# Optimization experiments

Measured on AMD Instinct MI355X. Metric: run time of the kernel, lower is better.

The kernel has to match this reference:

```python
import jax, jax.numpy as jnp
import numpy as np

D_MODEL = 1024
N_HEADS = 16
D_HEAD = D_MODEL // N_HEADS
RANK = 128
KNOW_RANK = 128
N_COMPRESS = 64
N_EXPAND = 32
N_KNOW = 16384
TOPK_C = 8
TOPK_E = 4
KNOW_K = 8
B, S = 8, 1024
EPS_LN = 1e-5


def setup_inputs() -> dict:
    key = jax.random.key(0)
    ks = jax.random.split(key, 16)
    inp = {
        'x': jax.random.normal(ks[0], (B, S, D_MODEL), jnp.float32),
        'importance': jax.random.uniform(ks[1], (B, S), jnp.float32),
        # routers, stored as [d_model, n] so out = x @ W
        'Wc': jax.random.normal(ks[2], (D_MODEL, N_COMPRESS), jnp.float32) * 0.02,
        'WQr': jax.random.normal(ks[3], (D_MODEL, N_EXPAND), jnp.float32) * 0.02,
        'WKr': jax.random.normal(ks[4], (D_MODEL, N_EXPAND), jnp.float32) * 0.02,
        'WVr': jax.random.normal(ks[5], (D_MODEL, N_EXPAND), jnp.float32) * 0.02,
        'Wm': jax.random.normal(ks[6], (D_MODEL, N_COMPRESS), jnp.float32) * 0.02,
        # shared neuron pools
        'compress_neurons': jax.random.normal(ks[7], (N_COMPRESS, D_MODEL, RANK), jnp.float32) / np.sqrt(D_MODEL),
        'expand_pool': jax.random.normal(ks[8], (N_EXPAND, RANK, D_MODEL), jnp.float32) / np.sqrt(RANK),
        'knowledge_K': jax.random.normal(ks[9], (N_KNOW, KNOW_RANK), jnp.float32) * 0.02,
        'knowledge_V': jax.random.normal(ks[10], (N_KNOW, D_MODEL), jnp.float32) * 0.02,
        # output projection stored as [d_in, d_out]
        'W_O': jax.random.normal(ks[11], (D_MODEL, D_MODEL), jnp.float32) / np.sqrt(D_MODEL),
        'ln1_s': jnp.ones((D_MODEL,), jnp.float32),
        'ln1_b': jnp.zeros((D_MODEL,), jnp.float32),
        'ln2_s': jnp.ones((D_MODEL,), jnp.float32),
        'ln2_b': jnp.zeros((D_MODEL,), jnp.float32),
    }
    return inp


def _layernorm(x, s, b):
    mu = jnp.mean(x, axis=-1, keepdims=True)
    var = jnp.mean(jnp.square(x - mu), axis=-1, keepdims=True)
    return (x - mu) * jax.lax.rsqrt(var + EPS_LN) * s + b


def _topk_sparsify(w, k):
    # w: [B, n] -> sparse renormalized weights [B, n]
    vals, idx = jax.lax.top_k(w, k)
    rows = jnp.arange(w.shape[0])[:, None]
    sparse = jnp.zeros_like(w).at[rows, idx].set(vals)
    return sparse / (jnp.sum(sparse, axis=-1, keepdims=True) + 1e-8)


def _route(nx, importance, W, k):
    pref = jax.nn.softmax(jnp.einsum('bsd,dn->bsn', nx, W), axis=-1)
    dense = jnp.einsum('bs,bsn->bn', importance, pref)
    return _topk_sparsify(dense, k)


def _forward(x, importance, Wc, WQr, WKr, WVr, Wm, compress_neurons,
             expand_pool, knowledge_K, knowledge_V, W_O, ln1_s, ln1_b, ln2_s, ln2_b):
    Bx, Sx, D = x.shape
    n1 = _layernorm(x, ln1_s, ln1_b)

    # --- attention routing ---
    cw = _route(n1, importance, Wc, TOPK_C)
    ewQ = _route(n1, importance, WQr, TOPK_E)
    ewK = _route(n1, importance, WKr, TOPK_E)
    ewV = _route(n1, importance, WVr, TOPK_E)

    # --- synthesized low-rank attention weights ---
    shared_compress = jnp.einsum('bn,ndr->bdr', cw, compress_neurons)
    h = jnp.einsum('bsd,bdr->bsr', n1, shared_compress)
    EQ = jnp.einsum('bn,nrd->brd', ewQ, expand_pool)
    EK = jnp.einsum('bn,nrd->brd', ewK, expand_pool)
    EV = jnp.einsum('bn,nrd->brd', ewV, expand_pool)
    Q = jnp.einsum('bsr,brd->bsd', h, EQ).reshape(Bx, Sx, N_HEADS, D_HEAD).transpose(0, 2, 1, 3)
    K = jnp.einsum('bsr,brd->bsd', h, EK).reshape(Bx, Sx, N_HEADS, D_HEAD).transpose(0, 2, 1, 3)
    V = jnp.einsum('bsr,brd->bsd', h, EV).reshape(Bx, Sx, N_HEADS, D_HEAD).transpose(0, 2, 1, 3)

    scores = jnp.einsum('bhqd,bhkd->bhqk', Q, K) / np.sqrt(D_HEAD)
    causal = jnp.tril(jnp.ones((Sx, Sx), bool))
    scores = jnp.where(causal, scores, jnp.finfo(scores.dtype).min)
    attn = jax.nn.softmax(scores, axis=-1)
    attn_out = jnp.einsum('bhqk,bhkd->bhqd', attn, V).transpose(0, 2, 1, 3).reshape(Bx, Sx, D)
    attn_out = attn_out @ W_O
    x = x + attn_out

    # --- memory ---
    n2 = _layernorm(x, ln2_s, ln2_b)
    mw = _route(n2, importance, Wm, TOPK_C)
    sc_m = jnp.einsum('bn,ndr->bdr', mw, compress_neurons)
    Qm = jnp.einsum('bsd,bdr->bsr', n2, sc_m)  # knowledge_rank == rank -> no query_proj
    mscores = jnp.einsum('bsr,nr->bsn', Qm, knowledge_K) / np.sqrt(KNOW_RANK)
    topv, topi = jax.lax.top_k(mscores, KNOW_K)
    w = jax.nn.softmax(topv, axis=-1)  # [B,S,k]
    selV = knowledge_V[topi]  # [B,S,k,D]
    mem_out = jnp.einsum('bsk,bskd->bsd', w, selV)
    return x + mem_out


def reference(x, importance, Wc, WQr, WKr, WVr, Wm, compress_neurons,
              expand_pool, knowledge_K, knowledge_V, W_O, ln1_s, ln1_b, ln2_s, ln2_b):
    return _forward(x, importance, Wc, WQr, WKr, WVr, Wm, compress_neurons,
                    expand_pool, knowledge_K, knowledge_V, W_O, ln1_s, ln1_b, ln2_s, ln2_b)
```

## Files before the change

kernel.cpp:

```cpp
#include <hip/hip_runtime.h>
#include <hip/hip_bf16.h>

#define BD 8
#define SD 1024
#define DM 1024
#define NH 16
#define DH 64
#define RK 128
#define NK 16384

typedef __attribute__((ext_vector_type(8))) short bf16x8;
typedef __attribute__((ext_vector_type(4))) float f32x4;

__device__ __forceinline__ unsigned short f2b(float f) {
    unsigned u = __float_as_uint(f);
    unsigned r = (u + 0x7FFFu + ((u >> 16) & 1u)) >> 16;
    return (unsigned short)r;
}
__device__ __forceinline__ float b2f(unsigned short h) {
    return __uint_as_float(((unsigned)h) << 16);
}

__global__ void __launch_bounds__(256) ln_kernel(const float* __restrict__ x,
                                                 const float* __restrict__ sc,
                                                 const float* __restrict__ bi,
                                                 unsigned short* __restrict__ outh,
                                                 unsigned short* __restrict__ outl) {
    const int tok = blockIdx.x;
    __shared__ float xs[DM];
    __shared__ float red[256];
    const float* xp = x + (size_t)tok * DM;
    float s = 0.f;
    for (int i = threadIdx.x; i < DM; i += 256) { float v = xp[i]; xs[i] = v; s += v; }
    red[threadIdx.x] = s; __syncthreads();
    for (int st = 128; st; st >>= 1) { if (threadIdx.x < st) red[threadIdx.x] += red[threadIdx.x + st]; __syncthreads(); }
    float mu = red[0] * (1.f / DM);
    __syncthreads();
    float vs = 0.f;
    for (int i = threadIdx.x; i < DM; i += 256) { float d = xs[i] - mu; vs += d * d; }
    red[threadIdx.x] = vs; __syncthreads();
    for (int st = 128; st; st >>= 1) { if (threadIdx.x < st) red[threadIdx.x] += red[threadIdx.x + st]; __syncthreads(); }
    float rs = rsqrtf(red[0] * (1.f / DM) + 1e-5f);
    for (int i = threadIdx.x; i < DM; i += 256) {
        float v = (xs[i] - mu) * rs * sc[i] + bi[i];
        unsigned short h = f2b(v);
        outh[(size_t)tok * DM + i] = h;
        outl[(size_t)tok * DM + i] = f2b(v - b2f(h));
    }
}

__global__ void __launch_bounds__(256) concatw_kernel(const float* __restrict__ Wc,
                                                      const float* __restrict__ WQr,
                                                      const float* __restrict__ WKr,
                                                      const float* __restrict__ WVr,
                                                      const float* __restrict__ Wm,
                                                      unsigned short* __restrict__ WTh,
                                                      unsigned short* __restrict__ WTl) {
    const int i = blockIdx.x * 256 + threadIdx.x;
    const int c = i >> 10, d = i & 1023;
    float v = 0.f;
    if (c < 64)       v = Wc[d * 64 + c];
    else if (c < 96)  v = WQr[d * 32 + c - 64];
    else if (c < 128) v = WKr[d * 32 + c - 96];
    else if (c < 160) v = WVr[d * 32 + c - 128];
    else if (c >= 192) v = Wm[d * 64 + c - 192];
    unsigned short h = f2b(v);
    WTh[i] = h;
    WTl[i] = f2b(v - b2f(h));
}

__global__ void __launch_bounds__(256) gemm_split(const unsigned short* __restrict__ Ah,
                                                  const unsigned short* __restrict__ Al,
                                                  const unsigned short* __restrict__ Bh,
                                                  const unsigned short* __restrict__ Bl,
                                                  float* __restrict__ C,
                                                  int N, int K) {
    const int row0 = blockIdx.y * 128, col0 = blockIdx.x * 64;
    const int t = threadIdx.x;
    const int w = t >> 6, l = t & 63, lq = l & 15, lg = l >> 4;
    __shared__ unsigned short sAh[128 * 64];
    __shared__ unsigned short sAl[128 * 64];
    __shared__ unsigned short sBh[64 * 64];
    __shared__ unsigned short sBl[64 * 64];
    f32x4 acc[2][4];
    #pragma unroll
    for (int mi = 0; mi < 2; mi++)
        #pragma unroll
        for (int ni = 0; ni < 4; ni++) acc[mi][ni] = f32x4{0.f, 0.f, 0.f, 0.f};

    for (int k0 = 0; k0 < K; k0 += 64) {
        __syncthreads();
        #pragma unroll
        for (int p = 0; p < 4; p++) {
            const int e = t * 8 + p * 2048;
            const int row = e >> 6, col = e & 63;
            const int sw = (e * 2) ^ ((row & 7) << 4);
            *(bf16x8*)((char*)sAh + sw) = *(const bf16x8*)(Ah + (size_t)(row0 + row) * K + k0 + col);
            *(bf16x8*)((char*)sAl + sw) = *(const bf16x8*)(Al + (size_t)(row0 + row) * K + k0 + col);
        }
        #pragma unroll
        for (int p = 0; p < 2; p++) {
            const int e = t * 8 + p * 2048;
            const int row = e >> 6, col = e & 63;
            const int sw = (e * 2) ^ ((row & 7) << 4);
            *(bf16x8*)((char*)sBh + sw) = *(const bf16x8*)(Bh + (size_t)(col0 + row) * K + k0 + col);
            *(bf16x8*)((char*)sBl + sw) = *(const bf16x8*)(Bl + (size_t)(col0 + row) * K + k0 + col);
        }
        __syncthreads();
        #pragma unroll
        for (int kk = 0; kk < 2; kk++) {
            bf16x8 ah[2], al[2], bh[4], bl[4];
            #pragma unroll
            for (int mi = 0; mi < 2; mi++) {
                const int r = w * 32 + mi * 16 + lq;
                const int off = (r * 128 + lg * 16 + kk * 64) ^ ((r & 7) << 4);
                ah[mi] = *(const bf16x8*)((const char*)sAh + off);
                al[mi] = *(const bf16x8*)((const char*)sAl + off);
            }
            #pragma unroll
            for (int ni = 0; ni < 4; ni++) {
                const int r = ni * 16 + lq;
                const int off = (r * 128 + lg * 16 + kk * 64) ^ ((r & 7) << 4);
                bh[ni] = *(const bf16x8*)((const char*)sBh + off);
                bl[ni] = *(const bf16x8*)((const char*)sBl + off);
            }
            #pragma unroll
            for (int mi = 0; mi < 2; mi++)
                #pragma unroll
                for (int ni = 0; ni < 4; ni++) {
                    acc[mi][ni] = __builtin_amdgcn_mfma_f32_16x16x32_bf16(ah[mi], bh[ni], acc[mi][ni], 0, 0, 0);
                    acc[mi][ni] = __builtin_amdgcn_mfma_f32_16x16x32_bf16(ah[mi], bl[ni], acc[mi][ni], 0, 0, 0);
                    acc[mi][ni] = __builtin_amdgcn_mfma_f32_16x16x32_bf16(al[mi], bh[ni], acc[mi][ni], 0, 0, 0);
                }
        }
    }
    #pragma unroll
    for (int mi = 0; mi < 2; mi++)
        #pragma unroll
        for (int j = 0; j < 4; j++) {
            const int row = row0 + w * 32 + mi * 16 + lg * 4 + j;
            #pragma unroll
            for (int ni = 0; ni < 4; ni++)
                C[(size_t)row * N + col0 + ni * 16 + lq] = acc[mi][ni][j];
        }
}

__global__ void __launch_bounds__(256) softpref_kernel(const float* __restrict__ lgt,
                                                       const float* __restrict__ imp,
                                                       float* __restrict__ wpref) {
    const int tok = blockIdx.x * 64 + (threadIdx.x >> 2);
    const int sg = threadIdx.x & 3;
    const int o = (sg == 0) ? 0 : (64 + 32 * (sg - 1));
    const int n = (sg == 0) ? 64 : 32;
    const float* lp = lgt + (size_t)tok * 192 + o;
    float m = -1e30f;
    for (int i = 0; i < n; i++) m = fmaxf(m, lp[i]);
    float ss = 0.f;
    for (int i = 0; i < n; i++) ss += __expf(lp[i] - m);
    const float scl = imp[tok] / ss;
    float* wp = wpref + (size_t)tok * 160 + o;
    for (int i = 0; i < n; i++) wp[i] = __expf(lp[i] - m) * scl;
}

__global__ void __launch_bounds__(256) softm_kernel(const float* __restrict__ lgt,
                                                    const float* __restrict__ imp,
                                                    float* __restrict__ wpref) {
    const int tok = blockIdx.x * 256 + threadIdx.x;
    const float* lp = lgt + (size_t)tok * 64;
    float m = -1e30f;
    for (int i = 0; i < 64; i++) m = fmaxf(m, lp[i]);
    float ss = 0.f;
    for (int i = 0; i < 64; i++) ss += __expf(lp[i] - m);
    const float scl = imp[tok] / ss;
    for (int i = 0; i < 64; i++) wpref[(size_t)tok * 64 + i] = __expf(lp[i] - m) * scl;
}

__global__ void __launch_bounds__(256) reduce_pref(const float* __restrict__ wpref,
                                                   float* __restrict__ dense,
                                                   int ncols, int outoff) {
    const int b = blockIdx.x / ncols, c = blockIdx.x % ncols;
    __shared__ float red[256];
    float s = 0.f;
    for (int si = threadIdx.x; si < SD; si += 256)
        s += wpref[((size_t)(b * SD + si)) * ncols + c];
    red[threadIdx.x] = s; __syncthreads();
    for (int st = 128; st; st >>= 1) { if (threadIdx.x < st) red[threadIdx.x] += red[threadIdx.x + st]; __syncthreads(); }
    if (threadIdx.x == 0) dense[b * 224 + outoff + c] = red[0];
}

__global__ void topk_kernel(const float* __restrict__ dense,
                            int* __restrict__ ridx, float* __restrict__ rw,
                            int r0, int nr) {
    const int t = threadIdx.x;
    if (t >= BD * nr) return;
    const int b = t / nr, r = r0 + (t % nr);
    const int offs[5] = {0, 64, 96, 128, 160};
    const int ns[5]   = {64, 32, 32, 32, 64};
    const int ks[5]   = {8, 4, 4, 4, 8};
    const float* dv = dense + b * 224 + offs[r];
    const int n = ns[r], k = ks[r];
    unsigned long long mask = 0;
    float vals[8]; int idxs[8];
    float ssum = 0.f;
    for (int kk = 0; kk < k; kk++) {
        float best = -1e30f; int bi = 0;
        for (int i = 0; i < n; i++)
            if (!((mask >> i) & 1ull) && dv[i] > best) { best = dv[i]; bi = i; }
        mask |= 1ull << bi;
        vals[kk] = best; idxs[kk] = bi; ssum += best;
    }
    float inv = 1.f / (ssum + 1e-8f);
    for (int kk = 0; kk < 8; kk++) {
        ridx[(b * 5 + r) * 8 + kk] = (kk < k) ? idxs[kk] : 0;
        rw[(b * 5 + r) * 8 + kk]   = (kk < k) ? vals[kk] * inv : 0.f;
    }
}

__global__ void __launch_bounds__(256) combine_t_kernel(const float* __restrict__ pool,
                                                        const int* __restrict__ ridx,
                                                        const float* __restrict__ rw,
                                                        int router, int kc,
                                                        unsigned short* __restrict__ outT,
                                                        int Rp, int Cp) {
    const int b = blockIdx.z;
    const int r0 = blockIdx.y * 64, c0 = blockIdx.x * 64;
    __shared__ float ls[64][65];
    const int* ii = ridx + (b * 5 + router) * 8;
    const float* ww = rw + (b * 5 + router) * 8;
    const int t = threadIdx.x;
    const int rr = t >> 4, cc = (t & 15) * 4;
    #pragma unroll
    for (int p = 0; p < 4; p++) {
        const int r = rr + p * 16;
        float4 acc = {0.f, 0.f, 0.f, 0.f};
        for (int kk = 0; kk < kc; kk++) {
            const float w = ww[kk];
            float4 v = *(const float4*)&pool[((size_t)ii[kk] * Rp + r0 + r) * Cp + c0 + cc];
            acc.x += w * v.x; acc.y += w * v.y; acc.z += w * v.z; acc.w += w * v.w;
        }
        ls[r][cc] = acc.x; ls[r][cc + 1] = acc.y; ls[r][cc + 2] = acc.z; ls[r][cc + 3] = acc.w;
    }
    __syncthreads();
    unsigned short* op = outT + (size_t)b * Rp * Cp;
    #pragma unroll
    for (int q = 0; q < 2; q++) {
        const int c = (t >> 3) + q * 32;
        const int r8 = (t & 7) * 8;
        union { unsigned short s[8]; bf16x8 v; } u;
        #pragma unroll
        for (int j = 0; j < 8; j++) u.s[j] = f2b(ls[r8 + j][c]);
        *(bf16x8*)(op + (size_t)(c0 + c) * Rp + r0 + r8) = u.v;
    }
}

__global__ void __launch_bounds__(256) tcvt_kernel(const float* __restrict__ src,
                                                   unsigned short* __restrict__ dst,
                                                   int R, int Cc) {
    __shared__ float ls[64][65];
    const int r0 = blockIdx.y * 64, c0 = blockIdx.x * 64;
    const int t = threadIdx.x;
    #pragma unroll
    for (int p = 0; p < 16; p++) {
        const int e = p * 256 + t;
        const int r = e >> 6, c = e & 63;
        ls[r][c] = src[(size_t)(r0 + r) * Cc + c0 + c];
    }
    __syncthreads();
    #pragma unroll
    for (int p = 0; p < 16; p++) {
        const int e = p * 256 + t;
        const int c = e >> 6, r = e & 63;
        dst[(size_t)(c0 + c) * R + r0 + r] = f2b(ls[r][c]);
    }
}

__global__ void __launch_bounds__(256) cvt_bf16_kernel(const float* __restrict__ src,
                                                       unsigned short* __restrict__ dst,
                                                       float scale, int n4) {
    const int i = blockIdx.x * 256 + threadIdx.x;
    if (i >= n4) return;
    float4 v = ((const float4*)src)[i];
    unsigned r0 = (unsigned)f2b(v.x * scale) | ((unsigned)f2b(v.y * scale) << 16);
    unsigned r1 = (unsigned)f2b(v.z * scale) | ((unsigned)f2b(v.w * scale) << 16);
    uint2 o; o.x = r0; o.y = r1;
    ((uint2*)dst)[i] = o;
}

template<int OUTB, int HASX>
__global__ void __launch_bounds__(256) gemm_bf16(const unsigned short* __restrict__ A,
                                                 const unsigned short* __restrict__ Bt,
                                                 const float* __restrict__ X,
                                                 void* __restrict__ Cv,
                                                 int M, int N, int K,
                                                 long long sA, long long sB, long long sC) {
    const int bz = blockIdx.z;
    const unsigned short* Ab = A + (size_t)bz * sA;
    const unsigned short* Btb = Bt + (size_t)bz * sB;
    const int row0 = blockIdx.y * 128, col0 = blockIdx.x * 128;
    const int t = threadIdx.x;
    const int w = t >> 6, l = t & 63, lq = l & 15, lg = l >> 4;
    const int wr = w >> 1, wc = w & 1;
    __shared__ unsigned short As[128 * 64];
    __shared__ unsigned short Bs[128 * 64];
    f32x4 acc[4][4];
    #pragma unroll
    for (int mi = 0; mi < 4; mi++)
        #pragma unroll
        for (int ni = 0; ni < 4; ni++) acc[mi][ni] = f32x4{0.f, 0.f, 0.f, 0.f};

    for (int k0 = 0; k0 < K; k0 += 64) {
        __syncthreads();
        #pragma unroll
        for (int p = 0; p < 4; p++) {
            const int e = t * 8 + p * 2048;
            const int row = e >> 6, col = e & 63;
            bf16x8 va = *(const bf16x8*)(Ab + (size_t)(row0 + row) * K + k0 + col);
            *(bf16x8*)((char*)As + ((row * 128 + col * 2) ^ ((row & 7) << 4))) = va;
            bf16x8 vb = *(const bf16x8*)(Btb + (size_t)(col0 + row) * K + k0 + col);
            *(bf16x8*)((char*)Bs + ((row * 128 + col * 2) ^ ((row & 7) << 4))) = vb;
        }
        __syncthreads();
        #pragma unroll
        for (int kk = 0; kk < 2; kk++) {
            bf16x8 af[4], bg[4];
            #pragma unroll
            for (int mi = 0; mi < 4; mi++) {
                const int r = wr * 64 + mi * 16 + lq;
                af[mi] = *(const bf16x8*)((const char*)As + ((r * 128 + lg * 16 + kk * 64) ^ ((r & 7) << 4)));
            }
            #pragma unroll
            for (int ni = 0; ni < 4; ni++) {
                const int r = wc * 64 + ni * 16 + lq;
                bg[ni] = *(const bf16x8*)((const char*)Bs + ((r * 128 + lg * 16 + kk * 64) ^ ((r & 7) << 4)));
            }
            #pragma unroll
            for (int mi = 0; mi < 4; mi++)
                #pragma unroll
                for (int ni = 0; ni < 4; ni++)
                    acc[mi][ni] = __builtin_amdgcn_mfma_f32_16x16x32_bf16(af[mi], bg[ni], acc[mi][ni], 0, 0, 0);
        }
    }
    #pragma unroll
    for (int mi = 0; mi < 4; mi++) {
        #pragma unroll
        for (int j = 0; j < 4; j++) {
            const int row = row0 + wr * 64 + mi * 16 + lg * 4 + j;
            #pragma unroll
            for (int ni = 0; ni < 4; ni++) {
                const int col = col0 + wc * 64 + ni * 16 + lq;
                float v = acc[mi][ni][j];
                if (HASX) v += X[(size_t)row * N + col];
                if (OUTB) ((unsigned short*)Cv)[(size_t)bz * sC + (size_t)row * N + col] = f2b(v);
                else      ((float*)Cv)[(size_t)bz * sC + (size_t)row * N + col] = v;
            }
        }
    }
}

#define SWZV(d) (((((d) >> 1) ^ ((d) >> 3)) & 7) << 4)
__global__ void __launch_bounds__(256) attn_mfma_kernel(const unsigned short* __restrict__ Q,
                                                        const unsigned short* __restrict__ K,
                                                        const unsigned short* __restrict__ V,
                                                        unsigned short* __restrict__ O) {
    const int qt = blockIdx.x, hh = blockIdx.y, b = blockIdx.z;
    const int t = threadIdx.x;
    const int w = t >> 6, l = t & 63, lq = l & 15, lg = l >> 4;

    __shared__ unsigned short ks[2][64 * 64];
    __shared__ unsigned short vt[2][64 * 64];
    __shared__ unsigned short pl[4][16 * 64];

    const size_t base = (size_t)b * SD * DM + (size_t)hh * DH;
    const int qA = qt;
    const int qB = 15 - qt;

    bf16x8 aqA[2], aqB[2];
    {
        const unsigned short* qp = Q + base + (size_t)(qA * 64 + w * 16 + lq) * DM + lg * 8;
        aqA[0] = *(const bf16x8*)qp; aqA[1] = *(const bf16x8*)(qp + 32);
        const unsigned short* qp2 = Q + base + (size_t)(qB * 64 + w * 16 + lq) * DM + lg * 8;
        aqB[0] = *(const bf16x8*)qp2; aqB[1] = *(const bf16x8*)(qp2 + 32);
    }

    f32x4 oA[4], oB[4];
    #pragma unroll
    for (int dt = 0; dt < 4; dt++) { oA[dt] = f32x4{0.f,0.f,0.f,0.f}; oB[dt] = f32x4{0.f,0.f,0.f,0.f}; }
    float mA[4] = {-1e30f,-1e30f,-1e30f,-1e30f}, sA[4] = {0.f,0.f,0.f,0.f};
    float mB[4] = {-1e30f,-1e30f,-1e30f,-1e30f}, sB[4] = {0.f,0.f,0.f,0.f};

    const int ntile = 16 - qt;
    const int srow = t >> 3;
    const int scol = (t & 7) * 8;

    int cur = 0;

    #pragma unroll
    for (int p = 0; p < 2; p++) {
        const int row = srow + 32 * p;
        bf16x8 kv = *(const bf16x8*)(K + base + (size_t)row * DM + scol);
        *(bf16x8*)((char*)&ks[0][0] + ((row * 128 + scol * 2) ^ ((row & 7) << 4))) = kv;
        bf16x8 vv = *(const bf16x8*)(V + base + (size_t)row * DM + scol);
        #pragma unroll
        for (int j2 = 0; j2 < 8; j2++) {
            const int d = scol + j2;
            *(unsigned short*)((char*)&vt[0][0] + ((d * 128 + row * 2) ^ SWZV(d))) = (unsigned short)vv[j2];
        }
    }
    __syncthreads();

    auto compute = [&](int q0, const bf16x8* aq, f32x4* o_, float* m_, float* s_, int kt) {
        const f32x4 zero4 = {0.f, 0.f, 0.f, 0.f};
        f32x4 sacc[4];
        #pragma unroll
        for (int ct = 0; ct < 4; ct++) {
            const int krow = ct * 16 + lq;
            bf16x8 b0 = *(const bf16x8*)((const char*)&ks[cur][0] + ((krow * 128 + lg * 16) ^ ((lq & 7) << 4)));
            bf16x8 b1 = *(const bf16x8*)((const char*)&ks[cur][0] + ((krow * 128 + lg * 16 + 64) ^ ((lq & 7) << 4)));
            f32x4 s = __builtin_amdgcn_mfma_f32_16x16x32_bf16(aq[0], b0, zero4, 0, 0, 0);
            s = __builtin_amdgcn_mfma_f32_16x16x32_bf16(aq[1], b1, s, 0, 0, 0);
            sacc[ct] = s;
        }
        float tm[4];
        #pragma unroll
        for (int j = 0; j < 4; j++) {
            const int qg = q0 * 64 + w * 16 + lg * 4 + j;
            float mx = -1e30f;
            #pragma unroll
            for (int ct = 0; ct < 4; ct++) {
                const int kg = kt * 64 + ct * 16 + lq;
                float v = sacc[ct][j] * 0.125f;
                v = (kg <= qg) ? v : -1e30f;
                sacc[ct][j] = v;
                mx = fmaxf(mx, v);
            }
            #pragma unroll
            for (int d = 1; d < 16; d <<= 1) mx = fmaxf(mx, __shfl_xor(mx, d));
            tm[j] = mx;
        }
        #pragma unroll
        for (int j = 0; j < 4; j++) {
            const float nm = fmaxf(m_[j], tm[j]);
            const float so = __expf(m_[j] - nm);
            m_[j] = nm;
            float rs = 0.f;
            const int prow = lg * 4 + j;
            #pragma unroll
            for (int ct = 0; ct < 4; ct++) {
                const float p = __expf(sacc[ct][j] - nm);
                rs += p;
                const int byteoff = ((prow * 128) + (ct * 16 + lq) * 2) ^ ((prow & 7) << 4);
                *(unsigned short*)((char*)&pl[w][0] + byteoff) = f2b(p);
            }
            #pragma unroll
            for (int d = 1; d < 16; d <<= 1) rs += __shfl_xor(rs, d);
            s_[j] = s_[j] * so + rs;
            #pragma unroll
            for (int dt = 0; dt < 4; dt++) o_[dt][j] *= so;
        }
        asm volatile("s_waitcnt lgkmcnt(0)" ::: "memory");
        __builtin_amdgcn_sched_barrier(0);
        #pragma unroll
        for (int c = 0; c < 2; c++) {
            bf16x8 pa = *(const bf16x8*)((const char*)&pl[w][0] +
                          ((lq * 128 + lg * 16 + 64 * c) ^ ((lq & 7) << 4)));
            #pragma unroll
            for (int dt = 0; dt < 4; dt++) {
                const int dd = dt * 16 + lq;
                bf16x8 bv = *(const bf16x8*)((const char*)&vt[cur][0] +
                              ((dd * 128 + lg * 16 + 64 * c) ^ SWZV(dd)));
                o_[dt] = __builtin_amdgcn_mfma_f32_16x16x32_bf16(pa, bv, o_[dt], 0, 0, 0);
            }
        }
    };

    const int mymaxA = qA * 64 + w * 16 + 15;
    for (int kt = 0; kt < ntile; kt++) {
        bf16x8 kN[2], vN[2];
        const bool pre = (kt + 1 < ntile);
        if (pre) {
            #pragma unroll
            for (int p = 0; p < 2; p++) {
                const int row = srow + 32 * p;
                kN[p] = *(const bf16x8*)(K + base + (size_t)((kt + 1) * 64 + row) * DM + scol);
                vN[p] = *(const bf16x8*)(V + base + (size_t)((kt + 1) * 64 + row) * DM + scol);
            }
        }
        compute(qB, aqB, oB, mB, sB, kt);
        if (kt * 64 <= mymaxA) compute(qA, aqA, oA, mA, sA, kt);
        if (pre) {
            #pragma unroll
            for (int p = 0; p < 2; p++) {
                const int row = srow + 32 * p;
                *(bf16x8*)((char*)&ks[cur ^ 1][0] + ((row * 128 + scol * 2) ^ ((row & 7) << 4))) = kN[p];
                #pragma unroll
                for (int j2 = 0; j2 < 8; j2++) {
                    const int d = scol + j2;
                    *(unsigned short*)((char*)&vt[cur ^ 1][0] + ((d * 128 + row * 2) ^ SWZV(d))) =
                        (unsigned short)vN[p][j2];
                }
            }
        }
        __syncthreads();
        cur ^= 1;
    }

    #pragma unroll
    for (int j = 0; j < 4; j++) {
        const float invA = 1.f / sA[j];
        const float invB = 1.f / sB[j];
        const int rowA = qA * 64 + w * 16 + lg * 4 + j;
        const int rowB = qB * 64 + w * 16 + lg * 4 + j;
        unsigned short* opA = O + base + (size_t)rowA * DM;
        unsigned short* opB = O + base + (size_t)rowB * DM;
        #pragma unroll
        for (int dt = 0; dt < 4; dt++) {
            opA[dt * 16 + lq] = f2b(oA[dt][j] * invA);
            opB[dt * 16 + lq] = f2b(oB[dt][j] * invB);
        }
    }
}
#undef SWZV

#define CE(a, b) { float hi_ = fmaxf(a, b), lo_ = fminf(a, b); a = hi_; b = lo_; }
__global__ void __launch_bounds__(512, 4) know_score_kernel(const unsigned short* __restrict__ Qmb,
                                                            const unsigned short* __restrict__ kKb,
                                                            float* __restrict__ cand) {
    const int t = threadIdx.x;
    const int w = t >> 6, l = t & 63, lq = l & 15, lg = l >> 4;
    const int tok0 = blockIdx.x * 16;
    __shared__ unsigned short ks[8][16 * 128];

    bf16x8 aq[4];
    {
        const unsigned short* qp = Qmb + (size_t)(tok0 + lq) * 128 + lg * 8;
        #pragma unroll
        for (int c = 0; c < 4; c++) aq[c] = *(const bf16x8*)(qp + c * 32);
    }

    float L[4][8];
    #pragma unroll
    for (int j = 0; j < 4; j++)
        #pragma unroll
        for (int s = 0; s < 8; s++) L[j][s] = __uint_as_float(0xF2000000u | (unsigned)s);

    const unsigned short* gsrc = kKb + (((size_t)w * 2048) << 7) + l * 8;
    unsigned short* myks = &ks[w][0];

    bf16x8 vreg[4];
    #pragma unroll
    for (int p = 0; p < 4; p++) vreg[p] = *(const bf16x8*)(gsrc + p * 512);

    for (int t4 = 0; t4 < 32; t4++) {
        float B[4][4];
        #pragma unroll
        for (int sub = 0; sub < 4; sub++) {
            const int kt = t4 * 4 + sub;
            #pragma unroll
            for (int p = 0; p < 4; p++) {
                const int e = p * 512 + l * 8;
                const int row = e >> 7;
                *(bf16x8*)((char*)myks + ((e * 2) ^ ((row & 7) << 4))) = vreg[p];
            }
            if (kt < 127) {
                const unsigned short* src2 = gsrc + (size_t)(kt + 1) * 2048;
                #pragma unroll
                for (int p = 0; p < 4; p++) vreg[p] = *(const bf16x8*)(src2 + p * 512);
            }
            {
                const char* kb = (const char*)myks + lq * 256;
                const int sw = (lq & 7) << 4;
                f32x4 s = {0.f, 0.f, 0.f, 0.f};
                #pragma unroll
                for (int c = 0; c < 4; c++) {
                    bf16x8 bv = *(const bf16x8*)(kb + ((c * 64 + lg * 16) ^ sw));
                    s = __builtin_amdgcn_mfma_f32_16x16x32_bf16(aq[c], bv, s, 0, 0, 0);
                }
                const unsigned keyb = (unsigned)(w * 2048 + kt * 16 + lq);
                #pragma unroll
                for (int j = 0; j < 4; j++) {
                    unsigned u = __float_as_uint(s[j]);
                    B[j][sub] = __uint_as_float((u & 0xFFFFC000u) | keyb);
                }
            }
        }
        #pragma unroll
        for (int j = 0; j < 4; j++) {
            CE(B[j][0], B[j][2]); CE(B[j][1], B[j][3]);
            CE(B[j][0], B[j][1]); CE(B[j][2], B[j][3]);
            CE(B[j][1], B[j][2]);
            L[j][4] = fmaxf(L[j][4], B[j][3]);
            L[j][5] = fmaxf(L[j][5], B[j][2]);
            L[j][6] = fmaxf(L[j][6], B[j][1]);
            L[j][7] = fmaxf(L[j][7], B[j][0]);
            CE(L[j][0], L[j][4]); CE(L[j][1], L[j][5]); CE(L[j][2], L[j][6]); CE(L[j][3], L[j][7]);
            CE(L[j][0], L[j][2]); CE(L[j][1], L[j][3]); CE(L[j][4], L[j][6]); CE(L[j][5], L[j][7]);
            CE(L[j][0], L[j][1]); CE(L[j][2], L[j][3]); CE(L[j][4], L[j][5]); CE(L[j][6], L[j][7]);
        }
    }
    #pragma unroll
    for (int j = 0; j < 4; j++) {
        const int tok = tok0 + lg * 4 + j;
        float* cp = cand + ((size_t)tok << 10) + w * 128 + lq * 8;
        #pragma unroll
        for (int ss = 0; ss < 8; ss++) cp[ss] = L[j][ss];
    }
}
#undef CE

__global__ void __launch_bounds__(256) know_out_kernel(const float* __restrict__ cand,
                                                       const float* __restrict__ kV,
                                                       float* __restrict__ out) {
    const int t = threadIdx.x, w = t >> 6, l = t & 63;
    const int tok = blockIdx.x * 4 + w;
    const float* cp = cand + ((size_t)tok << 10);
    float lv[16];
    #pragma unroll
    for (int i = 0; i < 16; i++) lv[i] = cp[i * 64 + l];

    float topv[8]; int topi[8];
    #pragma unroll
    for (int kk = 0; kk < 8; kk++) {
        float m = lv[0];
        #pragma unroll
        for (int i = 1; i < 16; i++) m = fmaxf(m, lv[i]);
        #pragma unroll
        for (int d = 1; d < 64; d <<= 1) m = fmaxf(m, __shfl_xor(m, d));
        topv[kk] = m;
        topi[kk] = (int)(__float_as_uint(m) & 0x3FFFu);
        #pragma unroll
        for (int i = 0; i < 16; i++) lv[i] = (lv[i] == m) ? -1e31f : lv[i];
    }
    const float mx = topv[0];
    float e[8]; float ssum = 0.f;
    #pragma unroll
    for (int kk = 0; kk < 8; kk++) { e[kk] = __expf(topv[kk] - mx); ssum += e[kk]; }
    const float inv = 1.f / ssum;

    float4 acc[4];
    #pragma unroll
    for (int ch = 0; ch < 4; ch++) acc[ch] = float4{0.f, 0.f, 0.f, 0.f};
    #pragma unroll
    for (int kk = 0; kk < 8; kk++) {
        const float wk = e[kk] * inv;
        const float* vp = kV + ((size_t)topi[kk] << 10);
        #pragma unroll
        for (int ch = 0; ch < 4; ch++) {
            float4 v = *(const float4*)(vp + ch * 256 + l * 4);
            acc[ch].x += wk * v.x; acc[ch].y += wk * v.y;
            acc[ch].z += wk * v.z; acc[ch].w += wk * v.w;
        }
    }
    float* op = out + ((size_t)tok << 10);
    #pragma unroll
    for (int ch = 0; ch < 4; ch++) {
        float4 o = *(const float4*)(op + ch * 256 + l * 4);
        o.x += acc[ch].x; o.y += acc[ch].y; o.z += acc[ch].z; o.w += acc[ch].w;
        *(float4*)(op + ch * 256 + l * 4) = o;
    }
}

extern "C" void kernel_launch(void* const* d_in, const int* in_sizes, int n_in,
                              void* d_out, int out_size, void* d_ws, size_t ws_size,
                              hipStream_t stream) {
    const float* x    = (const float*)d_in[0];
    const float* imp  = (const float*)d_in[1];
    const float* Wc   = (const float*)d_in[2];
    const float* WQr  = (const float*)d_in[3];
    const float* WKr  = (const float*)d_in[4];
    const float* WVr  = (const float*)d_in[5];
    const float* Wm   = (const float*)d_in[6];
    const float* cneu = (const float*)d_in[7];
    const float* epool= (const float*)d_in[8];
    const float* kK   = (const float*)d_in[9];
    const float* kV   = (const float*)d_in[10];
    const float* WO   = (const float*)d_in[11];
    const float* ln1s = (const float*)d_in[12];
    const float* ln1b = (const float*)d_in[13];
    const float* ln2s = (const float*)d_in[14];
    const float* ln2b = (const float*)d_in[15];
    float* out = (float*)d_out;

    float* ws = (float*)d_ws;
    size_t o = 0;
    unsigned short* n1h = (unsigned short*)(ws + o); o += (size_t)BD * SD * DM / 2;
    unsigned short* n1l = (unsigned short*)(ws + o); o += (size_t)BD * SD * DM / 2;
    float* lgt   = ws + o; o += (size_t)BD * SD * 192;
    float* wpref = ws + o; o += (size_t)BD * SD * 160;
    float* dense = ws + o; o += (size_t)BD * 224;
    int*   ridx  = (int*)(ws + o); o += (size_t)BD * 5 * 8;
    float* rw    = ws + o; o += (size_t)BD * 5 * 8;
    unsigned short* WTh = (unsigned short*)(ws + o); o += (size_t)256 * 1024 / 2;
    unsigned short* WTl = (unsigned short*)(ws + o); o += (size_t)256 * 1024 / 2;
    unsigned short* scompT = (unsigned short*)(ws + o); o += (size_t)BD * RK * DM / 2;
    unsigned short* EQt = (unsigned short*)(ws + o); o += (size_t)BD * RK * DM / 2;
    unsigned short* EKt = (unsigned short*)(ws + o); o += (size_t)BD * RK * DM / 2;
    unsigned short* EVt = (unsigned short*)(ws + o); o += (size_t)BD * RK * DM / 2;
    unsigned short* hb  = (unsigned short*)(ws + o); o += (size_t)BD * SD * RK / 2;
    unsigned short* Qb16 = (unsigned short*)(ws + o); o += (size_t)BD * SD * DM / 2;
    unsigned short* Kb16 = (unsigned short*)(ws + o); o += (size_t)BD * SD * DM / 2;
    unsigned short* Vb16 = (unsigned short*)(ws + o); o += (size_t)BD * SD * DM / 2;
    unsigned short* attnb = (unsigned short*)(ws + o); o += (size_t)BD * SD * DM / 2;
    unsigned short* WOt = (unsigned short*)(ws + o); o += (size_t)DM * DM / 2;
    unsigned short* kKb = (unsigned short*)(ws + o); o += (size_t)NK * RK / 2;
    unsigned short* Qmb = (unsigned short*)(ws + o); o += (size_t)BD * SD * RK / 2;
    float* cand = ws + o; o += (size_t)BD * SD * 1024;

    const int NTOK = BD * SD;

    concatw_kernel<<<1024, 256, 0, stream>>>(Wc, WQr, WKr, WVr, Wm, WTh, WTl);
    tcvt_kernel<<<dim3(16, 16, 1), 256, 0, stream>>>(WO, WOt, DM, DM);
    cvt_bf16_kernel<<<(NK * RK / 4) / 256, 256, 0, stream>>>(kK, kKb, 0.0883883476483184f, NK * RK / 4);

    ln_kernel<<<NTOK, 256, 0, stream>>>(x, ln1s, ln1b, n1h, n1l);
    gemm_split<<<dim3(3, NTOK / 128), 256, 0, stream>>>(n1h, n1l, WTh, WTl, lgt, 192, DM);
    softpref_kernel<<<NTOK / 64, 256, 0, stream>>>(lgt, imp, wpref);
    reduce_pref<<<BD * 160, 256, 0, stream>>>(wpref, dense, 160, 0);
    topk_kernel<<<1, 64, 0, stream>>>(dense, ridx, rw, 0, 4);
    combine_t_kernel<<<dim3(2, 16, BD), 256, 0, stream>>>(cneu, ridx, rw, 0, 8, scompT, DM, RK);
    combine_t_kernel<<<dim3(16, 2, BD), 256, 0, stream>>>(epool, ridx, rw, 1, 4, EQt, RK, DM);
    combine_t_kernel<<<dim3(16, 2, BD), 256, 0, stream>>>(epool, ridx, rw, 2, 4, EKt, RK, DM);
    combine_t_kernel<<<dim3(16, 2, BD), 256, 0, stream>>>(epool, ridx, rw, 3, 4, EVt, RK, DM);
    gemm_bf16<1, 0><<<dim3(1, 8, BD), 256, 0, stream>>>(n1h, scompT, nullptr, hb,
        SD, RK, DM, (long long)SD * DM, (long long)RK * DM, (long long)SD * RK);
    gemm_bf16<1, 0><<<dim3(8, 8, BD), 256, 0, stream>>>(hb, EQt, nullptr, Qb16,
        SD, DM, RK, (long long)SD * RK, (long long)DM * RK, (long long)SD * DM);
    gemm_bf16<1, 0><<<dim3(8, 8, BD), 256, 0, stream>>>(hb, EKt, nullptr, Kb16,
        SD, DM, RK, (long long)SD * RK, (long long)DM * RK, (long long)SD * DM);
    gemm_bf16<1, 0><<<dim3(8, 8, BD), 256, 0, stream>>>(hb, EVt, nullptr, Vb16,
        SD, DM, RK, (long long)SD * RK, (long long)DM * RK, (long long)SD * DM);
    attn_mfma_kernel<<<dim3(8, NH, BD), 256, 0, stream>>>(Qb16, Kb16, Vb16, attnb);
    gemm_bf16<0, 1><<<dim3(8, 64, 1), 256, 0, stream>>>(attnb, WOt, x, out,
        NTOK, DM, DM, 0, 0, 0);

    ln_kernel<<<NTOK, 256, 0, stream>>>(out, ln2s, ln2b, n1h, n1l);
    gemm_split<<<dim3(1, NTOK / 128), 256, 0, stream>>>(n1h, n1l,
        WTh + (size_t)192 * 1024, WTl + (size_t)192 * 1024, lgt, 64, DM);
    softm_kernel<<<NTOK / 256, 256, 0, stream>>>(lgt, imp, wpref);
    reduce_pref<<<BD * 64, 256, 0, stream>>>(wpref, dense, 64, 160);
    topk_kernel<<<1, 64, 0, stream>>>(dense, ridx, rw, 4, 1);
    combine_t_kernel<<<dim3(2, 16, BD), 256, 0, stream>>>(cneu, ridx, rw, 4, 8, scompT, DM, RK);
    gemm_bf16<1, 0><<<dim3(1, 8, BD), 256, 0, stream>>>(n1h, scompT, nullptr, Qmb,
        SD, RK, DM, (long long)SD * DM, (long long)RK * DM, (long long)SD * RK);
    know_score_kernel<<<NTOK / 16, 512, 0, stream>>>(Qmb, kKb, cand);
    know_out_kernel<<<NTOK / 4, 256, 0, stream>>>(cand, kV, out);
}
```

Measured before the change: 689.1 us.

## Fuse Q/K/V expand GEMMs into one and add narrow-tile GEMM for rank-128 projections

The three expand matrices are written side by side into one buffer, so a single batched GEMM produces an interleaved QKV tensor with a 3072-wide row stride. The attention kernel takes a leading-dimension argument to read from it. A dedicated 64x128-tile kernel replaces the generic GEMM for the two N=128 compress projections, giving 16 blocks per batch instead of 8. The aim is fewer launches and better occupancy on the skinny GEMMs, at the cost of strided Q/K/V reads in attention.

```diff
diff --git a/kernel.cpp b/kernel.cpp
--- a/kernel.cpp
+++ b/kernel.cpp
@@ -221,7 +221,7 @@
                                                         const float* __restrict__ rw,
                                                         int router, int kc,
                                                         unsigned short* __restrict__ outT,
-                                                        int Rp, int Cp) {
+                                                        int Rp, int Cp, long long sOut) {
     const int b = blockIdx.z;
     const int r0 = blockIdx.y * 64, c0 = blockIdx.x * 64;
     __shared__ float ls[64][65];
@@ -241,7 +241,7 @@
         ls[r][cc] = acc.x; ls[r][cc + 1] = acc.y; ls[r][cc + 2] = acc.z; ls[r][cc + 3] = acc.w;
     }
     __syncthreads();
-    unsigned short* op = outT + (size_t)b * Rp * Cp;
+    unsigned short* op = outT + (size_t)b * sOut;
     #pragma unroll
     for (int q = 0; q < 2; q++) {
         const int c = (t >> 3) + q * 32;
@@ -357,11 +357,67 @@
     }
 }
 
+__global__ void __launch_bounds__(256) gemm_h(const unsigned short* __restrict__ A,
+                                              const unsigned short* __restrict__ Bt,
+                                              unsigned short* __restrict__ C,
+                                              int K,
+                                              long long sA, long long sB, long long sC) {
+    const int bz = blockIdx.z;
+    const unsigned short* Ab = A + (size_t)bz * sA;
+    const unsigned short* Btb = Bt + (size_t)bz * sB;
+    const int row0 = blockIdx.y * 64;
+    const int t = threadIdx.x;
+    const int w = t >> 6, l = t & 63, lq = l & 15, lg = l >> 4;
+    __shared__ unsigned short As[64 * 64];
+    __shared__ unsigned short Bs[128 * 64];
+    f32x4 acc[8];
+    #pragma unroll
+    for (int ni = 0; ni < 8; ni++) acc[ni] = f32x4{0.f, 0.f, 0.f, 0.f};
+
+    for (int k0 = 0; k0 < K; k0 += 64) {
+        __syncthreads();
+        #pragma unroll
+        for (int p = 0; p < 2; p++) {
+            const int e = t * 8 + p * 2048;
+            const int row = e >> 6, col = e & 63;
+            bf16x8 va = *(const bf16x8*)(Ab + (size_t)(row0 + row) * K + k0 + col);
+            *(bf16x8*)((char*)As + ((row * 128 + col * 2) ^ ((row & 7) << 4))) = va;
+        }
+        #pragma unroll
+        for (int p = 0; p < 4; p++) {
+            const int e = t * 8 + p * 2048;
+            const int row = e >> 6, col = e & 63;
+            bf16x8 vb = *(const bf16x8*)(Btb + (size_t)row * K + k0 + col);
+            *(bf16x8*)((char*)Bs + ((row * 128 + col * 2) ^ ((row & 7) << 4))) = vb;
+        }
+        __syncthreads();
+        #pragma unroll
+        for (int kk = 0; kk < 2; kk++) {
+            const int ra = w * 16 + lq;
+            bf16x8 af = *(const bf16x8*)((const char*)As + ((ra * 128 + lg * 16 + kk * 64) ^ ((ra & 7) << 4)));
+            #pragma unroll
+            for (int ni = 0; ni < 8; ni++) {
+                const int r = ni * 16 + lq;
+                bf16x8 bg = *(const bf16x8*)((const char*)Bs + ((r * 128 + lg * 16 + kk * 64) ^ ((r & 7) << 4)));
+                acc[ni] = __builtin_amdgcn_mfma_f32_16x16x32_bf16(af, bg, acc[ni], 0, 0, 0);
+            }
+        }
+    }
+    #pragma unroll
+    for (int j = 0; j < 4; j++) {
+        const int row = row0 + w * 16 + lg * 4 + j;
+        #pragma unroll
+        for (int ni = 0; ni < 8; ni++)
+            C[(size_t)bz * sC + (size_t)row * 128 + ni * 16 + lq] = f2b(acc[ni][j]);
+    }
+}
+
 #define SWZV(d) (((((d) >> 1) ^ ((d) >> 3)) & 7) << 4)
 __global__ void __launch_bounds__(256) attn_mfma_kernel(const unsigned short* __restrict__ Q,
                                                         const unsigned short* __restrict__ K,
                                                         const unsigned short* __restrict__ V,
-                                                        unsigned short* __restrict__ O) {
+                                                        unsigned short* __restrict__ O,
+                                                        int ldq) {
     const int qt = blockIdx.x, hh = blockIdx.y, b = blockIdx.z;
     const int t = threadIdx.x;
     const int w = t >> 6, l = t & 63, lq = l & 15, lg = l >> 4;
@@ -370,15 +426,16 @@
     __shared__ unsigned short vt[2][64 * 64];
     __shared__ unsigned short pl[4][16 * 64];
 
-    const size_t base = (size_t)b * SD * DM + (size_t)hh * DH;
+    const size_t base = (size_t)b * SD * ldq + (size_t)hh * DH;
+    const size_t obase = (size_t)b * SD * DM + (size_t)hh * DH;
     const int qA = qt;
     const int qB = 15 - qt;
 
     bf16x8 aqA[2], aqB[2];
     {
-        const unsigned short* qp = Q + base + (size_t)(qA * 64 + w * 16 + lq) * DM + lg * 8;
+        const unsigned short* qp = Q + base + (size_t)(qA * 64 + w * 16 + lq) * ldq + lg * 8;
         aqA[0] = *(const bf16x8*)qp; aqA[1] = *(const bf16x8*)(qp + 32);
-        const unsigned short* qp2 = Q + base + (size_t)(qB * 64 + w * 16 + lq) * DM + lg * 8;
+        const unsigned short* qp2 = Q + base + (size_t)(qB * 64 + w * 16 + lq) * ldq + lg * 8;
         aqB[0] = *(const bf16x8*)qp2; aqB[1] = *(const bf16x8*)(qp2 + 32);
     }
 
@@ -397,9 +454,9 @@
     #pragma unroll
     for (int p = 0; p < 2; p++) {
         const int row = srow + 32 * p;
-        bf16x8 kv = *(const bf16x8*)(K + base + (size_t)row * DM + scol);
+        bf16x8 kv = *(const bf16x8*)(K + base + (size_t)row * ldq + scol);
         *(bf16x8*)((char*)&ks[0][0] + ((row * 128 + scol * 2) ^ ((row & 7) << 4))) = kv;
-        bf16x8 vv = *(const bf16x8*)(V + base + (size_t)row * DM + scol);
+        bf16x8 vv = *(const bf16x8*)(V + base + (size_t)row * ldq + scol);
         #pragma unroll
         for (int j2 = 0; j2 < 8; j2++) {
             const int d = scol + j2;
@@ -481,8 +538,8 @@
             #pragma unroll
             for (int p = 0; p < 2; p++) {
                 const int row = srow + 32 * p;
-                kN[p] = *(const bf16x8*)(K + base + (size_t)((kt + 1) * 64 + row) * DM + scol);
-                vN[p] = *(const bf16x8*)(V + base + (size_t)((kt + 1) * 64 + row) * DM + scol);
+                kN[p] = *(const bf16x8*)(K + base + (size_t)((kt + 1) * 64 + row) * ldq + scol);
+                vN[p] = *(const bf16x8*)(V + base + (size_t)((kt + 1) * 64 + row) * ldq + scol);
             }
         }
         compute(qB, aqB, oB, mB, sB, kt);
@@ -510,8 +567,8 @@
         const float invB = 1.f / sB[j];
         const int rowA = qA * 64 + w * 16 + lg * 4 + j;
         const int rowB = qB * 64 + w * 16 + lg * 4 + j;
-        unsigned short* opA = O + base + (size_t)rowA * DM;
-        unsigned short* opB = O + base + (size_t)rowB * DM;
+        unsigned short* opA = O + obase + (size_t)rowA * DM;
+        unsigned short* opB = O + obase + (size_t)rowB * DM;
         #pragma unroll
         for (int dt = 0; dt < 4; dt++) {
             opA[dt * 16 + lq] = f2b(oA[dt][j] * invA);
@@ -692,13 +749,9 @@
     unsigned short* WTh = (unsigned short*)(ws + o); o += (size_t)256 * 1024 / 2;
     unsigned short* WTl = (unsigned short*)(ws + o); o += (size_t)256 * 1024 / 2;
     unsigned short* scompT = (unsigned short*)(ws + o); o += (size_t)BD * RK * DM / 2;
-    unsigned short* EQt = (unsigned short*)(ws + o); o += (size_t)BD * RK * DM / 2;
-    unsigned short* EKt = (unsigned short*)(ws + o); o += (size_t)BD * RK * DM / 2;
-    unsigned short* EVt = (unsigned short*)(ws + o); o += (size_t)BD * RK * DM / 2;
+    unsigned short* E3t = (unsigned short*)(ws + o); o += (size_t)BD * 3 * DM * RK / 2;
     unsigned short* hb  = (unsigned short*)(ws + o); o += (size_t)BD * SD * RK / 2;
-    unsigned short* Qb16 = (unsigned short*)(ws + o); o += (size_t)BD * SD * DM / 2;
-    unsigned short* Kb16 = (unsigned short*)(ws + o); o += (size_t)BD * SD * DM / 2;
-    unsigned short* Vb16 = (unsigned short*)(ws + o); o += (size_t)BD * SD * DM / 2;
+    unsigned short* QKV16 = (unsigned short*)(ws + o); o += (size_t)BD * SD * 3072 / 2;
     unsigned short* attnb = (unsigned short*)(ws + o); o += (size_t)BD * SD * DM / 2;
     unsigned short* WOt = (unsigned short*)(ws + o); o += (size_t)DM * DM / 2;
     unsigned short* kKb = (unsigned short*)(ws + o); o += (size_t)NK * RK / 2;
@@ -706,6 +759,7 @@
     float* cand = ws + o; o += (size_t)BD * SD * 1024;
 
     const int NTOK = BD * SD;
+    const long long sE3 = (long long)3 * DM * RK;
 
     concatw_kernel<<<1024, 256, 0, stream>>>(Wc, WQr, WKr, WVr, Wm, WTh, WTl);
     tcvt_kernel<<<dim3(16, 16, 1), 256, 0, stream>>>(WO, WOt, DM, DM);
@@ -716,19 +770,20 @@
     softpref_kernel<<<NTOK / 64, 256, 0, stream>>>(lgt, imp, wpref);
     reduce_pref<<<BD * 160, 256, 0, stream>>>(wpref, dense, 160, 0);
     topk_kernel<<<1, 64, 0, stream>>>(dense, ridx, rw, 0, 4);
-    combine_t_kernel<<<dim3(2, 16, BD), 256, 0, stream>>>(cneu, ridx, rw, 0, 8, scompT, DM, RK);
-    combine_t_kernel<<<dim3(16, 2, BD), 256, 0, stream>>>(epool, ridx, rw, 1, 4, EQt, RK, DM);
-    combine_t_kernel<<<dim3(16, 2, BD), 256, 0, stream>>>(epool, ridx, rw, 2, 4, EKt, RK, DM);
-    combine_t_kernel<<<dim3(16, 2, BD), 256, 0, stream>>>(epool, ridx, rw, 3, 4, EVt, RK, DM);
-    gemm_bf16<1, 0><<<dim3(1, 8, BD), 256, 0, stream>>>(n1h, scompT, nullptr, hb,
-        SD, RK, DM, (long long)SD * DM, (long long)RK * DM, (long long)SD * RK);
-    gemm_bf16<1, 0><<<dim3(8, 8, BD), 256, 0, stream>>>(hb, EQt, nullptr, Qb16,
-        SD, DM, RK, (long long)SD * RK, (long long)DM * RK, (long long)SD * DM);
-    gemm_bf16<1, 0><<<dim3(8, 8, BD), 256, 0, stream>>>(hb, EKt, nullptr, Kb16,
-        SD, DM, RK, (long long)SD * RK, (long long)DM * RK, (long long)SD * DM);
-    gemm_bf16<1, 0><<<dim3(8, 8, BD), 256, 0, stream>>>(hb, EVt, nullptr, Vb16,
-        SD, DM, RK, (long long)SD * RK, (long long)DM * RK, (long long)SD * DM);
-    attn_mfma_kernel<<<dim3(8, NH, BD), 256, 0, stream>>>(Qb16, Kb16, Vb16, attnb);
+    combine_t_kernel<<<dim3(2, 16, BD), 256, 0, stream>>>(cneu, ridx, rw, 0, 8, scompT, DM, RK,
+        (long long)DM * RK);
+    combine_t_kernel<<<dim3(16, 2, BD), 256, 0, stream>>>(epool, ridx, rw, 1, 4,
+        E3t + (size_t)0 * DM * RK, RK, DM, sE3);
+    combine_t_kernel<<<dim3(16, 2, BD), 256, 0, stream>>>(epool, ridx, rw, 2, 4,
+        E3t + (size_t)1 * DM * RK, RK, DM, sE3);
+    combine_t_kernel<<<dim3(16, 2, BD), 256, 0, stream>>>(epool, ridx, rw, 3, 4,
+        E3t + (size_t)2 * DM * RK, RK, DM, sE3);
+    gemm_h<<<dim3(1, SD / 64, BD), 256, 0, stream>>>(n1h, scompT, hb,
+        DM, (long long)SD * DM, (long long)RK * DM, (long long)SD * RK);
+    gemm_bf16<1, 0><<<dim3(24, 8, BD), 256, 0, stream>>>(hb, E3t, nullptr, QKV16,
+        SD, 3072, RK, (long long)SD * RK, sE3, (long long)SD * 3072);
+    attn_mfma_kernel<<<dim3(8, NH, BD), 256, 0, stream>>>(QKV16, QKV16 + 1024, QKV16 + 2048,
+        attnb, 3072);
     gemm_bf16<0, 1><<<dim3(8, 64, 1), 256, 0, stream>>>(attnb, WOt, x, out,
         NTOK, DM, DM, 0, 0, 0);
 
@@ -738,9 +793,10 @@
     softm_kernel<<<NTOK / 256, 256, 0, stream>>>(lgt, imp, wpref);
     reduce_pref<<<BD * 64, 256, 0, stream>>>(wpref, dense, 64, 160);
     topk_kernel<<<1, 64, 0, stream>>>(dense, ridx, rw, 4, 1);
-    combine_t_kernel<<<dim3(2, 16, BD), 256, 0, stream>>>(cneu, ridx, rw, 4, 8, scompT, DM, RK);
-    gemm_bf16<1, 0><<<dim3(1, 8, BD), 256, 0, stream>>>(n1h, scompT, nullptr, Qmb,
-        SD, RK, DM, (long long)SD * DM, (long long)RK * DM, (long long)SD * RK);
+    combine_t_kernel<<<dim3(2, 16, BD), 256, 0, stream>>>(cneu, ridx, rw, 4, 8, scompT, DM, RK,
+        (long long)DM * RK);
+    gemm_h<<<dim3(1, SD / 64, BD), 256, 0, stream>>>(n1h, scompT, Qmb,
+        DM, (long long)SD * DM, (long long)RK * DM, (long long)SD * RK);
     know_score_kernel<<<NTOK / 16, 512, 0, stream>>>(Qmb, kKb, cand);
     know_out_kernel<<<NTOK / 4, 256, 0, stream>>>(cand, kV, out);
 }
```

Result: no change. 676.0 us (-1.9%).
